# Optimization experiments

Measured on AMD Instinct MI355X. Metric: run time of the kernel, lower is better.

The kernel has to match this reference:

```python
import jax, jax.numpy as jnp
import numpy as np

B, S, H, V, T, NS, NB, NSW = 16, 200, 400, 25000, 8, 30, 3, 36


def setup_inputs() -> dict:
    key = jax.random.key(0)
    ks = jax.random.split(key, 12)
    return {
        "encoded_hidden": jax.random.normal(ks[0], (1, B, H), jnp.float32),
        "encoded_outputs": jax.random.normal(ks[1], (B, S, H), jnp.float32),
        "story": jax.random.randint(ks[2], (B, S), 0, V),
        "target_batches": jax.random.randint(ks[3], (B, NS, T), 0, V),
        "slot_dom_idx": jax.random.randint(ks[4], (NS,), 0, NSW),
        "slot_slot_idx": jax.random.randint(ks[5], (NS,), 0, NSW),
        "emb_W": jax.random.normal(ks[6], (V, H), jnp.float32) * 0.05,
        "slot_emb_W": jax.random.normal(ks[7], (NSW, H), jnp.float32) * 0.1,
        "gru_W_ih": jax.random.normal(ks[8], (3 * H, H), jnp.float32) * 0.05,
        "gru_W_hh": jax.random.normal(ks[9], (3 * H, H), jnp.float32) * 0.05,
        "gru_b_ih": jnp.zeros((3 * H,), jnp.float32),
        "gru_b_hh": jnp.zeros((3 * H,), jnp.float32),
        "W_ratio_w": jax.random.normal(ks[10], (1, 3 * H), jnp.float32) * 0.05,
        "W_ratio_b": jnp.zeros((1,), jnp.float32),
        "W_gate_w": jax.random.normal(ks[11], (NB, H), jnp.float32) * 0.05,
        "W_gate_b": jnp.zeros((NB,), jnp.float32),
    }


def reference(encoded_hidden, encoded_outputs, story, target_batches,
              slot_dom_idx, slot_slot_idx, emb_W, slot_emb_W,
              gru_W_ih, gru_W_hh, gru_b_ih, gru_b_hh,
              W_ratio_w, W_ratio_b, W_gate_w, W_gate_b):
    b, s, h = encoded_outputs.shape
    ns = slot_dom_idx.shape[0]
    v = emb_W.shape[0]
    t = target_batches.shape[2]
    bs = ns * b  # flattened slot*batch dim (parallel decode over slots)

    # slot embedding = domain_emb + slot_emb, broadcast over batch
    slot_emb = slot_emb_W[slot_dom_idx] + slot_emb_W[slot_slot_idx]        # [ns,h]
    dec_in0 = jnp.broadcast_to(slot_emb[:, None, :], (ns, b, h)).reshape(bs, h)
    h0 = jnp.tile(encoded_hidden[0], (ns, 1))                              # [bs,h]
    enc = jnp.tile(encoded_outputs, (ns, 1, 1))                            # [bs,s,h]
    pad_mask = jnp.tile(story == 0, (ns, 1))                               # [bs,s]
    story_rep = jnp.tile(story, (ns, 1))                                   # [bs,s]
    # teacher forcing targets, slot-major flatten: [bs, t]
    tf = jnp.transpose(target_batches, (1, 0, 2)).reshape(bs, t)
    rows = jnp.arange(bs)

    def gru_cell(x, hid):
        gx = x @ gru_W_ih.T + gru_b_ih
        gh = hid @ gru_W_hh.T + gru_b_hh
        r = jax.nn.sigmoid(gx[:, :h] + gh[:, :h])
        z = jax.nn.sigmoid(gx[:, h:2 * h] + gh[:, h:2 * h])
        n = jnp.tanh(gx[:, 2 * h:] + r * gh[:, 2 * h:])
        return (1.0 - z) * n + z * hid

    def step(carry, tgt_t):
        hid, x = carry
        hid = gru_cell(x, hid)                                             # [bs,h]
        scores = jnp.einsum('bh,bsh->bs', hid, enc)
        scores = jnp.where(pad_mask, -jnp.inf, scores)
        prob = jax.nn.softmax(scores, axis=1)                              # [bs,s]
        ctx = jnp.einsum('bs,bsh->bh', prob, enc)                          # [bs,h]
        p_vocab = jax.nn.softmax(hid @ emb_W.T, axis=1)                    # [bs,v]
        switch = jax.nn.sigmoid(
            jnp.concatenate([hid, ctx, x], axis=-1) @ W_ratio_w.T + W_ratio_b)  # [bs,1]
        p_ctx = jnp.zeros((bs, v), p_vocab.dtype).at[rows[:, None], story_rep].add(prob)
        final = (1.0 - switch) * p_ctx + switch * p_vocab                  # [bs,v]
        x_next = emb_W[tgt_t]                                              # teacher forcing
        return (hid, x_next), (final, ctx)

    (_, _), (finals, ctxs) = jax.lax.scan(step, (h0, dec_in0), tf.T)
    all_point = jnp.transpose(finals.reshape(t, ns, b, v), (1, 2, 0, 3))   # [ns,b,t,v]
    all_gate = (ctxs[0] @ W_gate_w.T + W_gate_b).reshape(ns, b, -1)        # [ns,b,nb_gate]
    return all_point, all_gate
```

## Files before the change

### kernel.cpp

```cpp
#include <hip/hip_runtime.h>
#include <math.h>

#define B_   16
#define S_   200
#define H_   400
#define V_   25000
#define T_   8
#define NS_  30
#define NB_  3
#define NSW_ 36
#define BS_  480

#define KP_  448
#define MP_  512
#define NP_  25088
#define NG_  1280
#define MA_  3840
#define NVT_ (NP_/128)
#define PSL_ 200

typedef unsigned short u16;
typedef __attribute__((ext_vector_type(4))) float f32x4;
typedef __attribute__((ext_vector_type(8))) short short8;

__device__ __forceinline__ u16 f2bf(float f) {
    unsigned u = __float_as_uint(f);
    u += 0x7FFFu + ((u >> 16) & 1u);
    return (u16)(u >> 16);
}
__device__ __forceinline__ float bf2f(u16 v) {
    return __uint_as_float(((unsigned)v) << 16);
}
__device__ __forceinline__ float wred_sum(float v) {
    v += __shfl_xor(v, 32); v += __shfl_xor(v, 16); v += __shfl_xor(v, 8);
    v += __shfl_xor(v, 4);  v += __shfl_xor(v, 2);  v += __shfl_xor(v, 1);
    return v;
}
__device__ __forceinline__ float wred_max(float v) {
    v = fmaxf(v, __shfl_xor(v, 32)); v = fmaxf(v, __shfl_xor(v, 16));
    v = fmaxf(v, __shfl_xor(v, 8));  v = fmaxf(v, __shfl_xor(v, 4));
    v = fmaxf(v, __shfl_xor(v, 2));  v = fmaxf(v, __shfl_xor(v, 1));
    return v;
}

__device__ __forceinline__ void gload_lds16(const void* g, void* l) {
    __builtin_amdgcn_global_load_lds(
        (const __attribute__((address_space(1))) void*)g,
        (__attribute__((address_space(3))) void*)l, 16, 0, 0);
}

#define MFMA_SETUP()                                                          \
    const int wid = tid >> 6, lane = tid & 63;                                \
    const int wr = wid >> 1, wc = wid & 1;                                    \
    f32x4 acc[4][4] = {};                                                     \
    const int sslot = lane & 7;                                               \
    const int srow8 = (lane >> 3) & 7;                                        \
    const int lcol = (sslot ^ srow8) * 8;                                     \
    const int lr = lane & 15, lg = lane >> 4, lx = lane & 7;                  \
    const int sA0 = (lg ^ lx) * 8, sA1 = ((4 + lg) ^ lx) * 8;

#define STAGE_TILE(k0_)                                                       \
    {                                                                         \
        _Pragma("unroll")                                                     \
        for (int is = 0; is < 4; ++is) {                                      \
            gload_lds16(Ag + (size_t)is * 8 * KP_ + (k0_),                    \
                        &As[(wid * 32 + is * 8) * 64]);                       \
            gload_lds16(Bg + (size_t)is * 8 * KP_ + (k0_),                    \
                        &Bs[(wid * 32 + is * 8) * 64]);                       \
        }                                                                     \
    }

#define COMPUTE_TILE()                                                        \
    {                                                                         \
        short8 af[4][2], bfr[4][2];                                           \
        _Pragma("unroll")                                                     \
        for (int i = 0; i < 4; ++i) {                                         \
            int ra = (wr * 64 + i * 16 + lr) * 64;                            \
            af[i][0] = *reinterpret_cast<const short8*>(&As[ra + sA0]);       \
            af[i][1] = *reinterpret_cast<const short8*>(&As[ra + sA1]);       \
            int rb = (wc * 64 + i * 16 + lr) * 64;                            \
            bfr[i][0] = *reinterpret_cast<const short8*>(&Bs[rb + sA0]);      \
            bfr[i][1] = *reinterpret_cast<const short8*>(&Bs[rb + sA1]);      \
        }                                                                     \
        _Pragma("unroll")                                                     \
        for (int h = 0; h < 2; ++h)                                           \
            _Pragma("unroll")                                                 \
            for (int i = 0; i < 4; ++i)                                       \
                _Pragma("unroll")                                             \
                for (int j = 0; j < 4; ++j)                                   \
                    acc[i][j] = __builtin_amdgcn_mfma_f32_16x16x32_bf16(      \
                        af[i][h], bfr[j][h], acc[i][j], 0, 0, 0);             \
    }

#define MFMA_KLOOP_SB()                                                       \
    _Pragma("unroll")                                                         \
    for (int kt = 0; kt < 7; ++kt) {                                          \
        STAGE_TILE(kt * 64);                                                  \
        __syncthreads();                                                      \
        COMPUTE_TILE();                                                       \
        __syncthreads();                                                      \
    }

__global__ void init_all(const float* __restrict__ eh, float* __restrict__ hid,
                         u16* __restrict__ Ab) {
    int i = blockIdx.x * blockDim.x + threadIdx.x;
    if (i >= MP_ * KP_) return;
    int row = i / KP_, d = i - row * KP_;
    u16 v = 0;
    if (row < BS_ && d < H_) {
        float h = eh[(row % B_) * H_ + d];
        hid[row * H_ + d] = h;
        v = f2bf(h);
    }
    Ab[i] = v;
}

__device__ __forceinline__ void conv_chunk(const float* __restrict__ src,
                                           u16* __restrict__ dst, int i, int rows) {
    int row = i / (KP_ / 8), c8 = (i - row * (KP_ / 8)) * 8;
    short8 o = {};
    if (row < rows && c8 < H_) {
        const float4* s = reinterpret_cast<const float4*>(src + (size_t)row * H_ + c8);
        float4 a = s[0], b = s[1];
        o[0] = (short)f2bf(a.x); o[1] = (short)f2bf(a.y);
        o[2] = (short)f2bf(a.z); o[3] = (short)f2bf(a.w);
        o[4] = (short)f2bf(b.x); o[5] = (short)f2bf(b.y);
        o[6] = (short)f2bf(b.z); o[7] = (short)f2bf(b.w);
    }
    *reinterpret_cast<short8*>(dst + (size_t)row * KP_ + c8) = o;
}

__global__ void conv_all(const float* __restrict__ embW, const float* __restrict__ Wih,
                         const float* __restrict__ Whh, u16* __restrict__ Bb,
                         u16* __restrict__ Wihb, u16* __restrict__ Whhb) {
    const int CB = NP_ * (KP_ / 8), CG = NG_ * (KP_ / 8);
    int i = blockIdx.x * blockDim.x + threadIdx.x;
    if (i < CB) conv_chunk(embW, Bb, i, V_);
    else if (i < CB + CG) conv_chunk(Wih, Wihb, i - CB, 3 * H_);
    else if (i < CB + 2 * CG) conv_chunk(Whh, Whhb, i - CB - CG, 3 * H_);
}

__global__ void xall_prep(const int* __restrict__ tb, const float* __restrict__ embW,
                          const float* __restrict__ sembW,
                          const int* __restrict__ dom, const int* __restrict__ sli,
                          float* __restrict__ x_all, u16* __restrict__ Xb_all) {
    int i = blockIdx.x * blockDim.x + threadIdx.x;
    if (i >= MA_ * (KP_ / 8)) return;
    int row = i / (KP_ / 8), c8 = (i - row * (KP_ / 8)) * 8;
    int t = row / BS_, r = row - t * BS_;
    int batch = r % B_, slot = r / B_;
    short8 o = {};
    if (c8 < H_) {
        float4 a, b;
        if (t == 0) {
            const float4* s0 = reinterpret_cast<const float4*>(sembW + dom[slot] * H_ + c8);
            const float4* s1 = reinterpret_cast<const float4*>(sembW + sli[slot] * H_ + c8);
            float4 x0 = s0[0], x1 = s0[1], y0 = s1[0], y1 = s1[1];
            a = make_float4(x0.x + y0.x, x0.y + y0.y, x0.z + y0.z, x0.w + y0.w);
            b = make_float4(x1.x + y1.x, x1.y + y1.y, x1.z + y1.z, x1.w + y1.w);
        } else {
            int tok = tb[(batch * NS_ + slot) * T_ + (t - 1)];
            const float4* s = reinterpret_cast<const float4*>(embW + (size_t)tok * H_ + c8);
            a = s[0]; b = s[1];
        }
        o[0] = (short)f2bf(a.x); o[1] = (short)f2bf(a.y);
        o[2] = (short)f2bf(a.z); o[3] = (short)f2bf(a.w);
        o[4] = (short)f2bf(b.x); o[5] = (short)f2bf(b.y);
        o[6] = (short)f2bf(b.z); o[7] = (short)f2bf(b.w);
        *reinterpret_cast<float4*>(x_all + (size_t)row * H_ + c8) = a;
        *reinterpret_cast<float4*>(x_all + (size_t)row * H_ + c8 + 4) = b;
    }
    *reinterpret_cast<short8*>(Xb_all + (size_t)row * KP_ + c8) = o;
}

__global__ __launch_bounds__(256)
void gemm_setup(const u16* __restrict__ Xb_all, const u16* __restrict__ Abuf,
                const u16* __restrict__ Wihb, const u16* __restrict__ Whhb,
                float* __restrict__ gx_all, float* __restrict__ gh) {
    __shared__ u16 As[128 * 64];
    __shared__ u16 Bs[128 * 64];
    const int tid = threadIdx.x;
    const bool mainp = blockIdx.y < (MA_ / 128);
    const int m0 = (mainp ? blockIdx.y : blockIdx.y - MA_ / 128) * 128;
    const int n0 = blockIdx.x * 128;
    const u16* A = mainp ? Xb_all : Abuf;
    const u16* Bw = mainp ? Wihb : Whhb;
    float* C = mainp ? gx_all : gh;
    const int Mlim = mainp ? MA_ : BS_;

    MFMA_SETUP();
    const u16* Ag = A + (size_t)(m0 + wid * 32 + (lane >> 3)) * KP_ + lcol;
    const u16* Bg = Bw + (size_t)(n0 + wid * 32 + (lane >> 3)) * KP_ + lcol;
    MFMA_KLOOP_SB();

    const int m_base = m0 + wr * 64 + lg * 4;
    const int n_base = n0 + wc * 64 + lr;
    #pragma unroll
    for (int i = 0; i < 4; ++i)
        #pragma unroll
        for (int r = 0; r < 4; ++r) {
            int m = m_base + i * 16 + r;
            if (m >= Mlim) continue;
            #pragma unroll
            for (int j = 0; j < 4; ++j) {
                int n = n_base + j * 16;
                if (n < 3 * H_) C[(size_t)m * 3 * H_ + n] = acc[i][j][r];
            }
        }
}

__global__ __launch_bounds__(256, 2)
void vocab_gh(const u16* __restrict__ A, const u16* __restrict__ Bb,
              const u16* __restrict__ Whhb, u16* __restrict__ pb,
              float* __restrict__ psum, float* __restrict__ gh) {
    __shared__ u16 As[256 * 64];
    __shared__ u16 Bs[128 * 64];
    __shared__ float sred[2][256];
    const int bid = blockIdx.x;
    const int tid = threadIdx.x;
    const int xcd = bid & 7, idx = bid >> 3;
    const int lin = (xcd < 4) ? (xcd * 52 + idx) : (208 + (xcd - 4) * 51 + idx);
    const int ntall = lin >> 1, mt = lin & 1;
    const bool isv = (ntall < NVT_);
    const int n0 = (isv ? ntall : ntall - NVT_) * 128;
    const int m0 = mt * 256;
    const u16* Bsrc = isv ? Bb : Whhb;

    const int wid = tid >> 6, lane = tid & 63;
    const int wr = wid >> 1, wc = wid & 1;
    f32x4 acc[8][4] = {};
    const int sslot = lane & 7;
    const int srow8 = (lane >> 3) & 7;
    const int lcol = (sslot ^ srow8) * 8;
    const int lr = lane & 15, lg = lane >> 4, lx = lane & 7;
    const int sA0 = (lg ^ lx) * 8, sA1 = ((4 + lg) ^ lx) * 8;

    const u16* Ag = A + (size_t)(m0 + wid * 64 + (lane >> 3)) * KP_ + lcol;
    const u16* Bg = Bsrc + (size_t)(n0 + wid * 32 + (lane >> 3)) * KP_ + lcol;

    for (int kt = 0; kt < 7; ++kt) {
        const int k0 = kt * 64;
        #pragma unroll
        for (int is = 0; is < 8; ++is)
            gload_lds16(Ag + (size_t)is * 8 * KP_ + k0, &As[(wid * 64 + is * 8) * 64]);
        #pragma unroll
        for (int is = 0; is < 4; ++is)
            gload_lds16(Bg + (size_t)is * 8 * KP_ + k0, &Bs[(wid * 32 + is * 8) * 64]);
        __syncthreads();
        #pragma unroll
        for (int h = 0; h < 2; ++h) {
            const int sA = h ? sA1 : sA0;
            short8 af[8], bf[4];
            #pragma unroll
            for (int i = 0; i < 8; ++i)
                af[i] = *reinterpret_cast<const short8*>(&As[(wr * 128 + i * 16 + lr) * 64 + sA]);
            #pragma unroll
            for (int j = 0; j < 4; ++j)
                bf[j] = *reinterpret_cast<const short8*>(&Bs[(wc * 64 + j * 16 + lr) * 64 + sA]);
            #pragma unroll
            for (int i = 0; i < 8; ++i)
                #pragma unroll
                for (int j = 0; j < 4; ++j)
                    acc[i][j] = __builtin_amdgcn_mfma_f32_16x16x32_bf16(
                        af[i], bf[j], acc[i][j], 0, 0, 0);
        }
        __syncthreads();
    }

    const int m_base = m0 + wr * 128 + lg * 4;
    const int n_base = n0 + wc * 64 + lr;
    if (isv) {
        #pragma unroll
        for (int i = 0; i < 8; ++i) {
            #pragma unroll
            for (int r = 0; r < 4; ++r) {
                int m = m_base + i * 16 + r;
                float js = 0.f;
                #pragma unroll
                for (int j = 0; j < 4; ++j) {
                    int n = n_base + j * 16;
                    float e = __expf(acc[i][j][r]);
                    if (m < BS_ && n < V_) {
                        pb[(size_t)m * V_ + n] = f2bf(e);
                        js += e;
                    }
                }
                js += __shfl_xor(js, 1);
                js += __shfl_xor(js, 2);
                js += __shfl_xor(js, 4);
                js += __shfl_xor(js, 8);
                if ((lane & 15) == 0) sred[wc][m - m0] = js;
            }
        }
        __syncthreads();
        {
            int m = m0 + tid;
            psum[(size_t)m * PSL_ + ntall] = sred[0][tid] + sred[1][tid];
        }
    } else {
        #pragma unroll
        for (int i = 0; i < 8; ++i)
            #pragma unroll
            for (int r = 0; r < 4; ++r) {
                int m = m_base + i * 16 + r;
                if (m >= BS_) continue;
                #pragma unroll
                for (int j = 0; j < 4; ++j) {
                    int n = n_base + j * 16;
                    if (n < 3 * H_) gh[(size_t)m * 3 * H_ + n] = acc[i][j][r];
                }
            }
    }
}

__global__ __launch_bounds__(256)
void attn_fin(const float* __restrict__ gx_all, const float* __restrict__ gh,
              const float* __restrict__ bih, const float* __restrict__ bhh,
              float* __restrict__ hid, u16* __restrict__ Ab,
              const float* __restrict__ x_all,
              const float* __restrict__ enc, const int* __restrict__ story,
              const float* __restrict__ Wr, const float* __restrict__ Wrb,
              const float* __restrict__ Wg, const float* __restrict__ Wgb,
              float* __restrict__ prob_cur, float* __restrict__ sw_cur,
              float* __restrict__ gate_out,
              float* __restrict__ out, const u16* __restrict__ pb,
              const float* __restrict__ psum, const float* __restrict__ sw_prev,
              const float* __restrict__ prob_prev, int t) {
    const int bid = blockIdx.x;
    const int lin = (bid & 7) * 120 + (bid >> 3);
    const int work = lin >> 1, kind = lin & 1;
    const int tid = threadIdx.x, w = tid >> 6, l = tid & 63;
    __shared__ __align__(16) float hs[H_];
    __shared__ __align__(16) float xs[H_];
    __shared__ __align__(16) float cs[H_];
    __shared__ float sc[S_];
    __shared__ float red[16];

    if (kind == 1) {
        if (t == 0) return;
        const int row = work, batch = row % B_;
        float rs = (tid < NVT_) ? psum[(size_t)row * PSL_ + tid] : 0.f;
        rs = wred_sum(rs);
        if (l == 0) red[w] = rs;
        __syncthreads();
        float denom = red[0] + red[1] + red[2] + red[3];
        float swv = sw_prev[row];
        float scl = swv / denom;
        const u16* ps = pb + (size_t)row * V_;
        float* p = out + ((size_t)row * T_ + (t - 1)) * V_;
        for (int v = tid * 8; v < V_; v += 256 * 8) {
            short8 in = *reinterpret_cast<const short8*>(ps + v);
            float4 o0, o1;
            o0.x = bf2f((u16)in[0]) * scl; o0.y = bf2f((u16)in[1]) * scl;
            o0.z = bf2f((u16)in[2]) * scl; o0.w = bf2f((u16)in[3]) * scl;
            o1.x = bf2f((u16)in[4]) * scl; o1.y = bf2f((u16)in[5]) * scl;
            o1.z = bf2f((u16)in[6]) * scl; o1.w = bf2f((u16)in[7]) * scl;
            *reinterpret_cast<float4*>(p + v) = o0;
            *reinterpret_cast<float4*>(p + v + 4) = o1;
        }
        __syncthreads();
        float om = 1.f - swv;
        for (int s = tid; s < S_; s += 256) {
            int tok = story[batch * S_ + s];
            atomicAdd(p + tok, om * prob_prev[(size_t)row * S_ + s]);
        }
        return;
    }

    const int batch = work / 30, slot = work - batch * 30;
    const int row = slot * B_ + batch;

    const float* gxr = gx_all + ((size_t)t * BS_ + row) * 3 * H_;
    const float* ghr = gh + (size_t)row * 3 * H_;
    const float* xr  = x_all + ((size_t)t * BS_ + row) * H_;
    for (int d = tid; d < H_; d += 256) {
        float r = 1.f / (1.f + expf(-(gxr[d] + bih[d] + ghr[d] + bhh[d])));
        float z = 1.f / (1.f + expf(-(gxr[H_ + d] + bih[H_ + d] + ghr[H_ + d] + bhh[H_ + d])));
        float n = tanhf(gxr[2 * H_ + d] + bih[2 * H_ + d] + r * (ghr[2 * H_ + d] + bhh[2 * H_ + d]));
        float h = (1.f - z) * n + z * hid[(size_t)row * H_ + d];
        hs[d] = h;
        hid[(size_t)row * H_ + d] = h;
        Ab[(size_t)row * KP_ + d] = f2bf(h);
        xs[d] = xr[d];
    }
    __syncthreads();

    const float* encb = enc + (size_t)batch * S_ * H_;
    {
        float4 hv1 = *reinterpret_cast<const float4*>(&hs[l * 4]);
        float4 hv2 = make_float4(0.f, 0.f, 0.f, 0.f);
        if (l < 36) hv2 = *reinterpret_cast<const float4*>(&hs[256 + l * 4]);
        for (int k = 0; k < 50; ++k) {
            int s = w * 50 + k;
            const float4* e = reinterpret_cast<const float4*>(encb + (size_t)s * H_);
            float4 ev = e[l];
            float part = ev.x * hv1.x + ev.y * hv1.y + ev.z * hv1.z + ev.w * hv1.w;
            if (l < 36) {
                float4 ev2 = e[64 + l];
                part += ev2.x * hv2.x + ev2.y * hv2.y + ev2.z * hv2.z + ev2.w * hv2.w;
            }
            part = wred_sum(part);
            if (l == 0)
                sc[s] = (story[batch * S_ + s] == 0) ? -1e30f : part;
        }
    }
    __syncthreads();

    float v = (tid < S_) ? sc[tid] : -1e30f;
    float wm = wred_max(v);
    if (l == 0) red[w] = wm;
    __syncthreads();
    float mx = fmaxf(fmaxf(red[0], red[1]), fmaxf(red[2], red[3]));
    float e = (tid < S_) ? __expf(v - mx) : 0.f;
    float wsum = wred_sum(e);
    if (l == 0) red[4 + w] = wsum;
    __syncthreads();
    float inv = 1.f / (red[4] + red[5] + red[6] + red[7]);
    if (tid < S_) {
        float pv = e * inv;
        sc[tid] = pv;
        prob_cur[(size_t)row * S_ + tid] = pv;
    }
    __syncthreads();

    for (int d = tid; d < H_; d += 256) {
        float a0 = 0.f, a1 = 0.f;
        for (int s = 0; s < S_; s += 2) {
            a0 += sc[s] * encb[(size_t)s * H_ + d];
            a1 += sc[s + 1] * encb[(size_t)(s + 1) * H_ + d];
        }
        cs[d] = a0 + a1;
    }
    __syncthreads();

    float part = 0.f;
    for (int i = tid; i < 3 * H_; i += 256) {
        float xv = (i < H_) ? hs[i] : (i < 2 * H_) ? cs[i - H_] : xs[i - 2 * H_];
        part += xv * Wr[i];
    }
    part = wred_sum(part);
    if (l == 0) red[8 + w] = part;
    __syncthreads();
    if (tid == 0)
        sw_cur[row] = 1.f / (1.f + expf(-(red[8] + red[9] + red[10] + red[11] + Wrb[0])));

    if (t == 0 && tid < NB_) {
        float acc = 0.f;
        for (int d = 0; d < H_; ++d) acc += cs[d] * Wg[tid * H_ + d];
        gate_out[(size_t)row * NB_ + tid] = acc + Wgb[tid];
    }
}

__global__ __launch_bounds__(256)
void scale_scatter(float* __restrict__ out, const u16* __restrict__ pb,
                   const float* __restrict__ psum, const float* __restrict__ sw,
                   const float* __restrict__ prob, const int* __restrict__ story) {
    const int row = blockIdx.x;
    const int tid = threadIdx.x, w = tid >> 6, l = tid & 63;
    __shared__ float red[4];
    float rs = (tid < NVT_) ? psum[(size_t)row * PSL_ + tid] : 0.f;
    rs = wred_sum(rs);
    if (l == 0) red[w] = rs;
    __syncthreads();
    float denom = red[0] + red[1] + red[2] + red[3];
    float swv = sw[row];
    float scl = swv / denom;
    const u16* ps = pb + (size_t)row * V_;
    float* p = out + ((size_t)row * T_ + (T_ - 1)) * V_;
    for (int v = tid * 8; v < V_; v += 256 * 8) {
        short8 in = *reinterpret_cast<const short8*>(ps + v);
        float4 o0, o1;
        o0.x = bf2f((u16)in[0]) * scl; o0.y = bf2f((u16)in[1]) * scl;
        o0.z = bf2f((u16)in[2]) * scl; o0.w = bf2f((u16)in[3]) * scl;
        o1.x = bf2f((u16)in[4]) * scl; o1.y = bf2f((u16)in[5]) * scl;
        o1.z = bf2f((u16)in[6]) * scl; o1.w = bf2f((u16)in[7]) * scl;
        *reinterpret_cast<float4*>(p + v) = o0;
        *reinterpret_cast<float4*>(p + v + 4) = o1;
    }
    __syncthreads();
    const int batch = row % B_;
    float om = 1.f - swv;
    for (int s = tid; s < S_; s += 256) {
        int tok = story[batch * S_ + s];
        atomicAdd(p + tok, om * prob[(size_t)row * S_ + s]);
    }
}

extern "C" void kernel_launch(void* const* d_in, const int* in_sizes, int n_in,
                              void* d_out, int out_size, void* d_ws, size_t ws_size,
                              hipStream_t stream) {
    const float* eh    = (const float*)d_in[0];
    const float* enc   = (const float*)d_in[1];
    const int*   story = (const int*)d_in[2];
    const int*   tb    = (const int*)d_in[3];
    const int*   dom   = (const int*)d_in[4];
    const int*   sli   = (const int*)d_in[5];
    const float* embW  = (const float*)d_in[6];
    const float* sembW = (const float*)d_in[7];
    const float* Wih   = (const float*)d_in[8];
    const float* Whh   = (const float*)d_in[9];
    const float* bih   = (const float*)d_in[10];
    const float* bhh   = (const float*)d_in[11];
    const float* Wr    = (const float*)d_in[12];
    const float* Wrb   = (const float*)d_in[13];
    const float* Wg    = (const float*)d_in[14];
    const float* Wgb   = (const float*)d_in[15];

    float* out = (float*)d_out;
    float* ws  = (float*)d_ws;

    float* gx_all = ws;
    float* gh     = gx_all + (size_t)MA_ * 3 * H_;
    float* hid    = gh + (size_t)BS_ * 3 * H_;
    float* x_all  = hid + (size_t)BS_ * H_;
    float* prob2  = x_all + (size_t)MA_ * H_;
    float* sw2    = prob2 + 2 * BS_ * S_;
    float* psum   = sw2 + 2 * BS_;
    u16* Ab     = (u16*)(psum + (size_t)MP_ * PSL_);
    u16* Xb_all = Ab + (size_t)MP_ * KP_;
    u16* Wihb   = Xb_all + (size_t)MA_ * KP_;
    u16* Whhb   = Wihb + (size_t)NG_ * KP_;
    u16* Bb     = Whhb + (size_t)NG_ * KP_;
    u16* pb     = Bb + (size_t)NP_ * KP_;
    size_t need = (size_t)((char*)(pb + (size_t)BS_ * V_) - (char*)ws);
    if (ws_size < need) return;

    float* gate_out = out + (size_t)NS_ * B_ * T_ * V_;

    init_all<<<(MP_ * KP_ + 255) / 256, 256, 0, stream>>>(eh, hid, Ab);
    {
        int tot = (NP_ + 2 * NG_) * (KP_ / 8);
        conv_all<<<(tot + 255) / 256, 256, 0, stream>>>(embW, Wih, Whh, Bb, Wihb, Whhb);
    }
    xall_prep<<<(MA_ * (KP_ / 8) + 255) / 256, 256, 0, stream>>>(tb, embW, sembW, dom, sli,
                                                                 x_all, Xb_all);
    gemm_setup<<<dim3(NG_ / 128, MA_ / 128 + MP_ / 128), 256, 0, stream>>>(
        Xb_all, Ab, Wihb, Whhb, gx_all, gh);

    for (int t = 0; t < T_; ++t) {
        const int cur = t & 1, prev = cur ^ 1;
        attn_fin<<<960, 256, 0, stream>>>(gx_all, gh, bih, bhh, hid, Ab, x_all,
                                          enc, story, Wr, Wrb, Wg, Wgb,
                                          prob2 + cur * BS_ * S_, sw2 + cur * BS_,
                                          gate_out, out, pb, psum,
                                          sw2 + prev * BS_, prob2 + prev * BS_ * S_, t);
        vocab_gh<<<412, 256, 0, stream>>>(Ab, Bb, Whhb, pb, psum, gh);
    }
    {
        const int last = (T_ - 1) & 1;
        scale_scatter<<<BS_, 256, 0, stream>>>(out, pb, psum, sw2 + last * BS_,
                                               prob2 + last * BS_ * S_, story);
    }
}
```

Baseline: 777.9 us.

## Fuse decode loop into persistent cooperative kernel with grid syncs

Replaces the per-step attn_fin/vocab_gh launches with one cooperative persistent kernel that runs the setup GEMM, the attention step and the vocab GEMM, separated by grid-wide syncs. Setup conversion kernels are merged into one prep kernel. The finalize/scatter of the previous step now runs alongside the vocab GEMM using double-buffered pb/psum. The aim is to cut kernel launch overhead and idle tails between steps, at the cost of grid-sync latency and limited occupancy for 512 co-resident blocks. A non-cooperative fallback path keeps separate launches.

```diff
diff --git a/kernel.cpp b/kernel.cpp
--- a/kernel.cpp
+++ b/kernel.cpp
@@ -1,5 +1,8 @@
 #include <hip/hip_runtime.h>
+#include <hip/hip_cooperative_groups.h>
 #include <math.h>
+
+namespace cg = cooperative_groups;
 
 #define B_   16
 #define S_   200
@@ -8,7 +11,6 @@
 #define T_   8
 #define NS_  30
 #define NB_  3
-#define NSW_ 36
 #define BS_  480
 
 #define KP_  448
@@ -18,6 +20,8 @@
 #define MA_  3840
 #define NVT_ (NP_/128)
 #define PSL_ 200
+#define GRID_ 512
+#define SMEM_ 51200
 
 typedef unsigned short u16;
 typedef __attribute__((ext_vector_type(4))) float f32x4;
@@ -42,157 +46,62 @@
     v = fmaxf(v, __shfl_xor(v, 2));  v = fmaxf(v, __shfl_xor(v, 1));
     return v;
 }
-
 __device__ __forceinline__ void gload_lds16(const void* g, void* l) {
     __builtin_amdgcn_global_load_lds(
         (const __attribute__((address_space(1))) void*)g,
         (__attribute__((address_space(3))) void*)l, 16, 0, 0);
 }
 
-#define MFMA_SETUP()                                                          \
-    const int wid = tid >> 6, lane = tid & 63;                                \
-    const int wr = wid >> 1, wc = wid & 1;                                    \
-    f32x4 acc[4][4] = {};                                                     \
-    const int sslot = lane & 7;                                               \
-    const int srow8 = (lane >> 3) & 7;                                        \
-    const int lcol = (sslot ^ srow8) * 8;                                     \
-    const int lr = lane & 15, lg = lane >> 4, lx = lane & 7;                  \
-    const int sA0 = (lg ^ lx) * 8, sA1 = ((4 + lg) ^ lx) * 8;
-
-#define STAGE_TILE(k0_)                                                       \
-    {                                                                         \
-        _Pragma("unroll")                                                     \
-        for (int is = 0; is < 4; ++is) {                                      \
-            gload_lds16(Ag + (size_t)is * 8 * KP_ + (k0_),                    \
-                        &As[(wid * 32 + is * 8) * 64]);                       \
-            gload_lds16(Bg + (size_t)is * 8 * KP_ + (k0_),                    \
-                        &Bs[(wid * 32 + is * 8) * 64]);                       \
-        }                                                                     \
-    }
-
-#define COMPUTE_TILE()                                                        \
-    {                                                                         \
-        short8 af[4][2], bfr[4][2];                                           \
-        _Pragma("unroll")                                                     \
-        for (int i = 0; i < 4; ++i) {                                         \
-            int ra = (wr * 64 + i * 16 + lr) * 64;                            \
-            af[i][0] = *reinterpret_cast<const short8*>(&As[ra + sA0]);       \
-            af[i][1] = *reinterpret_cast<const short8*>(&As[ra + sA1]);       \
-            int rb = (wc * 64 + i * 16 + lr) * 64;                            \
-            bfr[i][0] = *reinterpret_cast<const short8*>(&Bs[rb + sA0]);      \
-            bfr[i][1] = *reinterpret_cast<const short8*>(&Bs[rb + sA1]);      \
-        }                                                                     \
-        _Pragma("unroll")                                                     \
-        for (int h = 0; h < 2; ++h)                                           \
-            _Pragma("unroll")                                                 \
-            for (int i = 0; i < 4; ++i)                                       \
-                _Pragma("unroll")                                             \
-                for (int j = 0; j < 4; ++j)                                   \
-                    acc[i][j] = __builtin_amdgcn_mfma_f32_16x16x32_bf16(      \
-                        af[i][h], bfr[j][h], acc[i][j], 0, 0, 0);             \
-    }
-
-#define MFMA_KLOOP_SB()                                                       \
-    _Pragma("unroll")                                                         \
-    for (int kt = 0; kt < 7; ++kt) {                                          \
-        STAGE_TILE(kt * 64);                                                  \
-        __syncthreads();                                                      \
-        COMPUTE_TILE();                                                       \
-        __syncthreads();                                                      \
-    }
-
-__global__ void init_all(const float* __restrict__ eh, float* __restrict__ hid,
-                         u16* __restrict__ Ab) {
-    int i = blockIdx.x * blockDim.x + threadIdx.x;
-    if (i >= MP_ * KP_) return;
-    int row = i / KP_, d = i - row * KP_;
-    u16 v = 0;
-    if (row < BS_ && d < H_) {
-        float h = eh[(row % B_) * H_ + d];
-        hid[row * H_ + d] = h;
-        v = f2bf(h);
-    }
-    Ab[i] = v;
-}
-
-__device__ __forceinline__ void conv_chunk(const float* __restrict__ src,
-                                           u16* __restrict__ dst, int i, int rows) {
-    int row = i / (KP_ / 8), c8 = (i - row * (KP_ / 8)) * 8;
-    short8 o = {};
-    if (row < rows && c8 < H_) {
-        const float4* s = reinterpret_cast<const float4*>(src + (size_t)row * H_ + c8);
-        float4 a = s[0], b = s[1];
-        o[0] = (short)f2bf(a.x); o[1] = (short)f2bf(a.y);
-        o[2] = (short)f2bf(a.z); o[3] = (short)f2bf(a.w);
-        o[4] = (short)f2bf(b.x); o[5] = (short)f2bf(b.y);
-        o[6] = (short)f2bf(b.z); o[7] = (short)f2bf(b.w);
-    }
-    *reinterpret_cast<short8*>(dst + (size_t)row * KP_ + c8) = o;
-}
-
-__global__ void conv_all(const float* __restrict__ embW, const float* __restrict__ Wih,
-                         const float* __restrict__ Whh, u16* __restrict__ Bb,
-                         u16* __restrict__ Wihb, u16* __restrict__ Whhb) {
-    const int CB = NP_ * (KP_ / 8), CG = NG_ * (KP_ / 8);
-    int i = blockIdx.x * blockDim.x + threadIdx.x;
-    if (i < CB) conv_chunk(embW, Bb, i, V_);
-    else if (i < CB + CG) conv_chunk(Wih, Wihb, i - CB, 3 * H_);
-    else if (i < CB + 2 * CG) conv_chunk(Whh, Whhb, i - CB - CG, 3 * H_);
-}
-
-__global__ void xall_prep(const int* __restrict__ tb, const float* __restrict__ embW,
-                          const float* __restrict__ sembW,
-                          const int* __restrict__ dom, const int* __restrict__ sli,
-                          float* __restrict__ x_all, u16* __restrict__ Xb_all) {
-    int i = blockIdx.x * blockDim.x + threadIdx.x;
-    if (i >= MA_ * (KP_ / 8)) return;
-    int row = i / (KP_ / 8), c8 = (i - row * (KP_ / 8)) * 8;
-    int t = row / BS_, r = row - t * BS_;
-    int batch = r % B_, slot = r / B_;
-    short8 o = {};
-    if (c8 < H_) {
-        float4 a, b;
-        if (t == 0) {
-            const float4* s0 = reinterpret_cast<const float4*>(sembW + dom[slot] * H_ + c8);
-            const float4* s1 = reinterpret_cast<const float4*>(sembW + sli[slot] * H_ + c8);
-            float4 x0 = s0[0], x1 = s0[1], y0 = s1[0], y1 = s1[1];
-            a = make_float4(x0.x + y0.x, x0.y + y0.y, x0.z + y0.z, x0.w + y0.w);
-            b = make_float4(x1.x + y1.x, x1.y + y1.y, x1.z + y1.z, x1.w + y1.w);
-        } else {
-            int tok = tb[(batch * NS_ + slot) * T_ + (t - 1)];
-            const float4* s = reinterpret_cast<const float4*>(embW + (size_t)tok * H_ + c8);
-            a = s[0]; b = s[1];
-        }
-        o[0] = (short)f2bf(a.x); o[1] = (short)f2bf(a.y);
-        o[2] = (short)f2bf(a.z); o[3] = (short)f2bf(a.w);
-        o[4] = (short)f2bf(b.x); o[5] = (short)f2bf(b.y);
-        o[6] = (short)f2bf(b.z); o[7] = (short)f2bf(b.w);
-        *reinterpret_cast<float4*>(x_all + (size_t)row * H_ + c8) = a;
-        *reinterpret_cast<float4*>(x_all + (size_t)row * H_ + c8 + 4) = b;
-    }
-    *reinterpret_cast<short8*>(Xb_all + (size_t)row * KP_ + c8) = o;
-}
-
-__global__ __launch_bounds__(256)
-void gemm_setup(const u16* __restrict__ Xb_all, const u16* __restrict__ Abuf,
-                const u16* __restrict__ Wihb, const u16* __restrict__ Whhb,
-                float* __restrict__ gx_all, float* __restrict__ gh) {
-    __shared__ u16 As[128 * 64];
-    __shared__ u16 Bs[128 * 64];
-    const int tid = threadIdx.x;
-    const bool mainp = blockIdx.y < (MA_ / 128);
-    const int m0 = (mainp ? blockIdx.y : blockIdx.y - MA_ / 128) * 128;
-    const int n0 = blockIdx.x * 128;
+__device__ __forceinline__ void setup_item(int item, const u16* Xb_all, const u16* Abuf,
+        const u16* Wihb, const u16* Whhb, float* gx_all, float* gh, char* smem, int tid) {
+    u16* As = (u16*)smem;
+    u16* Bs = (u16*)(smem + 16384);
+    const int nt = item % 10, mtile = item / 10;
+    const bool mainp = mtile < (MA_ / 128);
+    const int m0 = (mainp ? mtile : mtile - MA_ / 128) * 128;
+    const int n0 = nt * 128;
     const u16* A = mainp ? Xb_all : Abuf;
     const u16* Bw = mainp ? Wihb : Whhb;
     float* C = mainp ? gx_all : gh;
     const int Mlim = mainp ? MA_ : BS_;
 
-    MFMA_SETUP();
+    const int wid = tid >> 6, lane = tid & 63;
+    const int wr = wid >> 1, wc = wid & 1;
+    f32x4 acc[4][4] = {};
+    const int lcol = ((lane & 7) ^ ((lane >> 3) & 7)) * 8;
+    const int lr = lane & 15, lg = lane >> 4, lx = lane & 7;
+    const int sA0 = (lg ^ lx) * 8, sA1 = ((4 + lg) ^ lx) * 8;
     const u16* Ag = A + (size_t)(m0 + wid * 32 + (lane >> 3)) * KP_ + lcol;
     const u16* Bg = Bw + (size_t)(n0 + wid * 32 + (lane >> 3)) * KP_ + lcol;
-    MFMA_KLOOP_SB();
-
+
+    for (int kt = 0; kt < 7; ++kt) {
+        const int k0 = kt * 64;
+        #pragma unroll
+        for (int is = 0; is < 4; ++is) {
+            gload_lds16(Ag + (size_t)is * 8 * KP_ + k0, &As[(wid * 32 + is * 8) * 64]);
+            gload_lds16(Bg + (size_t)is * 8 * KP_ + k0, &Bs[(wid * 32 + is * 8) * 64]);
+        }
+        __syncthreads();
+        short8 af[4][2], bfr[4][2];
+        #pragma unroll
+        for (int i = 0; i < 4; ++i) {
+            int ra = (wr * 64 + i * 16 + lr) * 64;
+            af[i][0] = *reinterpret_cast<const short8*>(&As[ra + sA0]);
+            af[i][1] = *reinterpret_cast<const short8*>(&As[ra + sA1]);
+            int rb = (wc * 64 + i * 16 + lr) * 64;
+            bfr[i][0] = *reinterpret_cast<const short8*>(&Bs[rb + sA0]);
+            bfr[i][1] = *reinterpret_cast<const short8*>(&Bs[rb + sA1]);
+        }
+        #pragma unroll
+        for (int h = 0; h < 2; ++h)
+            #pragma unroll
+            for (int i = 0; i < 4; ++i)
+                #pragma unroll
+                for (int j = 0; j < 4; ++j)
+                    acc[i][j] = __builtin_amdgcn_mfma_f32_16x16x32_bf16(
+                        af[i][h], bfr[j][h], acc[i][j], 0, 0, 0);
+        __syncthreads();
+    }
     const int m_base = m0 + wr * 64 + lg * 4;
     const int n_base = n0 + wc * 64 + lr;
     #pragma unroll
@@ -209,16 +118,12 @@
         }
 }
 
-__global__ __launch_bounds__(256, 2)
-void vocab_gh(const u16* __restrict__ A, const u16* __restrict__ Bb,
-              const u16* __restrict__ Whhb, u16* __restrict__ pb,
-              float* __restrict__ psum, float* __restrict__ gh) {
-    __shared__ u16 As[256 * 64];
-    __shared__ u16 Bs[128 * 64];
-    __shared__ float sred[2][256];
-    const int bid = blockIdx.x;
-    const int tid = threadIdx.x;
-    const int xcd = bid & 7, idx = bid >> 3;
+__device__ __forceinline__ void vocab_item(int vbid, const u16* A, const u16* Bb,
+        const u16* Whhb, u16* pb, float* psum, float* gh, char* smem, int tid) {
+    u16* As = (u16*)smem;
+    u16* Bs = (u16*)(smem + 32768);
+    float (*sred)[256] = (float (*)[256])(smem + 49152);
+    const int xcd = vbid & 7, idx = vbid >> 3;
     const int lin = (xcd < 4) ? (xcd * 52 + idx) : (208 + (xcd - 4) * 51 + idx);
     const int ntall = lin >> 1, mt = lin & 1;
     const bool isv = (ntall < NVT_);
@@ -229,12 +134,9 @@
     const int wid = tid >> 6, lane = tid & 63;
     const int wr = wid >> 1, wc = wid & 1;
     f32x4 acc[8][4] = {};
-    const int sslot = lane & 7;
-    const int srow8 = (lane >> 3) & 7;
-    const int lcol = (sslot ^ srow8) * 8;
+    const int lcol = ((lane & 7) ^ ((lane >> 3) & 7)) * 8;
     const int lr = lane & 15, lg = lane >> 4, lx = lane & 7;
     const int sA0 = (lg ^ lx) * 8, sA1 = ((4 + lg) ^ lx) * 8;
-
     const u16* Ag = A + (size_t)(m0 + wid * 64 + (lane >> 3)) * KP_ + lcol;
     const u16* Bg = Bsrc + (size_t)(n0 + wid * 32 + (lane >> 3)) * KP_ + lcol;
 
@@ -313,62 +215,53 @@
     }
 }
 
-__global__ __launch_bounds__(256)
-void attn_fin(const float* __restrict__ gx_all, const float* __restrict__ gh,
-              const float* __restrict__ bih, const float* __restrict__ bhh,
-              float* __restrict__ hid, u16* __restrict__ Ab,
-              const float* __restrict__ x_all,
-              const float* __restrict__ enc, const int* __restrict__ story,
-              const float* __restrict__ Wr, const float* __restrict__ Wrb,
-              const float* __restrict__ Wg, const float* __restrict__ Wgb,
-              float* __restrict__ prob_cur, float* __restrict__ sw_cur,
-              float* __restrict__ gate_out,
-              float* __restrict__ out, const u16* __restrict__ pb,
-              const float* __restrict__ psum, const float* __restrict__ sw_prev,
-              const float* __restrict__ prob_prev, int t) {
-    const int bid = blockIdx.x;
-    const int lin = (bid & 7) * 120 + (bid >> 3);
-    const int work = lin >> 1, kind = lin & 1;
-    const int tid = threadIdx.x, w = tid >> 6, l = tid & 63;
-    __shared__ __align__(16) float hs[H_];
-    __shared__ __align__(16) float xs[H_];
-    __shared__ __align__(16) float cs[H_];
-    __shared__ float sc[S_];
-    __shared__ float red[16];
-
-    if (kind == 1) {
-        if (t == 0) return;
-        const int row = work, batch = row % B_;
-        float rs = (tid < NVT_) ? psum[(size_t)row * PSL_ + tid] : 0.f;
-        rs = wred_sum(rs);
-        if (l == 0) red[w] = rs;
-        __syncthreads();
-        float denom = red[0] + red[1] + red[2] + red[3];
-        float swv = sw_prev[row];
-        float scl = swv / denom;
-        const u16* ps = pb + (size_t)row * V_;
-        float* p = out + ((size_t)row * T_ + (t - 1)) * V_;
-        for (int v = tid * 8; v < V_; v += 256 * 8) {
-            short8 in = *reinterpret_cast<const short8*>(ps + v);
-            float4 o0, o1;
-            o0.x = bf2f((u16)in[0]) * scl; o0.y = bf2f((u16)in[1]) * scl;
-            o0.z = bf2f((u16)in[2]) * scl; o0.w = bf2f((u16)in[3]) * scl;
-            o1.x = bf2f((u16)in[4]) * scl; o1.y = bf2f((u16)in[5]) * scl;
-            o1.z = bf2f((u16)in[6]) * scl; o1.w = bf2f((u16)in[7]) * scl;
-            *reinterpret_cast<float4*>(p + v) = o0;
-            *reinterpret_cast<float4*>(p + v + 4) = o1;
-        }
-        __syncthreads();
-        float om = 1.f - swv;
-        for (int s = tid; s < S_; s += 256) {
-            int tok = story[batch * S_ + s];
-            atomicAdd(p + tok, om * prob_prev[(size_t)row * S_ + s]);
-        }
-        return;
-    }
-
-    const int batch = work / 30, slot = work - batch * 30;
+__device__ __forceinline__ void fin_row(int row, int tout, float* out, const u16* pb,
+        const float* psum, const float* sw, const float* prob, const int* story,
+        char* smem, int tid) {
+    float* red = (float*)smem;
+    const int w = tid >> 6, l = tid & 63;
+    const int batch = row % B_;
+    float rs = (tid < NVT_) ? psum[(size_t)row * PSL_ + tid] : 0.f;
+    rs = wred_sum(rs);
+    if (l == 0) red[w] = rs;
+    __syncthreads();
+    float denom = red[0] + red[1] + red[2] + red[3];
+    float swv = sw[row];
+    float scl = swv / denom;
+    const u16* ps = pb + (size_t)row * V_;
+    float* p = out + ((size_t)row * T_ + tout) * V_;
+    for (int v = tid * 8; v < V_; v += 256 * 8) {
+        short8 in = *reinterpret_cast<const short8*>(ps + v);
+        float4 o0, o1;
+        o0.x = bf2f((u16)in[0]) * scl; o0.y = bf2f((u16)in[1]) * scl;
+        o0.z = bf2f((u16)in[2]) * scl; o0.w = bf2f((u16)in[3]) * scl;
+        o1.x = bf2f((u16)in[4]) * scl; o1.y = bf2f((u16)in[5]) * scl;
+        o1.z = bf2f((u16)in[6]) * scl; o1.w = bf2f((u16)in[7]) * scl;
+        *reinterpret_cast<float4*>(p + v) = o0;
+        *reinterpret_cast<float4*>(p + v + 4) = o1;
+    }
+    __syncthreads();
+    float om = 1.f - swv;
+    for (int s = tid; s < S_; s += 256) {
+        int tok = story[batch * S_ + s];
+        atomicAdd(p + tok, om * prob[(size_t)row * S_ + s]);
+    }
+}
+
+__device__ __forceinline__ void attn_body(int abid, int t,
+        const float* gx_all, const float* gh, const float* bih, const float* bhh,
+        float* hid, u16* Ab, const float* x_all, const float* enc, const int* story,
+        const float* Wr, const float* Wrb, const float* Wg, const float* Wgb,
+        float* prob_cur, float* sw_cur, float* gate_out, char* smem, int tid) {
+    float* hs = (float*)smem;
+    float* xs = (float*)(smem + 1600);
+    float* cs = (float*)(smem + 3200);
+    float* sc = (float*)(smem + 4800);
+    float* red = (float*)(smem + 5600);
+    const int lin = (abid & 7) * 60 + (abid >> 3);
+    const int batch = lin / 30, slot = lin - batch * 30;
     const int row = slot * B_ + batch;
+    const int w = tid >> 6, l = tid & 63;
 
     const float* gxr = gx_all + ((size_t)t * BS_ + row) * 3 * H_;
     const float* ghr = gh + (size_t)row * 3 * H_;
@@ -449,41 +342,153 @@
         for (int d = 0; d < H_; ++d) acc += cs[d] * Wg[tid * H_ + d];
         gate_out[(size_t)row * NB_ + tid] = acc + Wgb[tid];
     }
-}
-
-__global__ __launch_bounds__(256)
-void scale_scatter(float* __restrict__ out, const u16* __restrict__ pb,
-                   const float* __restrict__ psum, const float* __restrict__ sw,
-                   const float* __restrict__ prob, const int* __restrict__ story) {
-    const int row = blockIdx.x;
-    const int tid = threadIdx.x, w = tid >> 6, l = tid & 63;
-    __shared__ float red[4];
-    float rs = (tid < NVT_) ? psum[(size_t)row * PSL_ + tid] : 0.f;
-    rs = wred_sum(rs);
-    if (l == 0) red[w] = rs;
-    __syncthreads();
-    float denom = red[0] + red[1] + red[2] + red[3];
-    float swv = sw[row];
-    float scl = swv / denom;
-    const u16* ps = pb + (size_t)row * V_;
-    float* p = out + ((size_t)row * T_ + (T_ - 1)) * V_;
-    for (int v = tid * 8; v < V_; v += 256 * 8) {
-        short8 in = *reinterpret_cast<const short8*>(ps + v);
-        float4 o0, o1;
-        o0.x = bf2f((u16)in[0]) * scl; o0.y = bf2f((u16)in[1]) * scl;
-        o0.z = bf2f((u16)in[2]) * scl; o0.w = bf2f((u16)in[3]) * scl;
-        o1.x = bf2f((u16)in[4]) * scl; o1.y = bf2f((u16)in[5]) * scl;
-        o1.z = bf2f((u16)in[6]) * scl; o1.w = bf2f((u16)in[7]) * scl;
-        *reinterpret_cast<float4*>(p + v) = o0;
-        *reinterpret_cast<float4*>(p + v + 4) = o1;
-    }
-    __syncthreads();
-    const int batch = row % B_;
-    float om = 1.f - swv;
-    for (int s = tid; s < S_; s += 256) {
-        int tok = story[batch * S_ + s];
-        atomicAdd(p + tok, om * prob[(size_t)row * S_ + s]);
-    }
+    __syncthreads();
+}
+
+__global__ void prep_all(const float* __restrict__ eh, const float* __restrict__ embW,
+                         const float* __restrict__ Wih, const float* __restrict__ Whh,
+                         const float* __restrict__ sembW, const int* __restrict__ tb,
+                         const int* __restrict__ dom, const int* __restrict__ sli,
+                         float* __restrict__ hid, u16* __restrict__ Ab,
+                         u16* __restrict__ Bb, u16* __restrict__ Wihb, u16* __restrict__ Whhb,
+                         float* __restrict__ x_all, u16* __restrict__ Xb_all) {
+    const int R0 = MP_ * KP_;
+    const int CB = NP_ * (KP_ / 8), CG = NG_ * (KP_ / 8);
+    const int R1 = R0 + CB + 2 * CG;
+    const int R2 = R1 + MA_ * (KP_ / 8);
+    int i = blockIdx.x * 256 + threadIdx.x;
+    if (i < R0) {
+        int row = i / KP_, d = i - row * KP_;
+        u16 v = 0;
+        if (row < BS_ && d < H_) {
+            float h = eh[(row % B_) * H_ + d];
+            hid[row * H_ + d] = h;
+            v = f2bf(h);
+        }
+        Ab[i] = v;
+    } else if (i < R1) {
+        int j = i - R0;
+        const float* src; u16* dst; int rows;
+        if (j < CB) { src = embW; dst = Bb; rows = V_; }
+        else if (j < CB + CG) { src = Wih; dst = Wihb; rows = 3 * H_; j -= CB; }
+        else { src = Whh; dst = Whhb; rows = 3 * H_; j -= CB + CG; }
+        int row = j / (KP_ / 8), c8 = (j - row * (KP_ / 8)) * 8;
+        short8 o = {};
+        if (row < rows && c8 < H_) {
+            const float4* s = reinterpret_cast<const float4*>(src + (size_t)row * H_ + c8);
+            float4 a = s[0], b = s[1];
+            o[0] = (short)f2bf(a.x); o[1] = (short)f2bf(a.y);
+            o[2] = (short)f2bf(a.z); o[3] = (short)f2bf(a.w);
+            o[4] = (short)f2bf(b.x); o[5] = (short)f2bf(b.y);
+            o[6] = (short)f2bf(b.z); o[7] = (short)f2bf(b.w);
+        }
+        *reinterpret_cast<short8*>(dst + (size_t)row * KP_ + c8) = o;
+    } else if (i < R2) {
+        int j = i - R1;
+        int row = j / (KP_ / 8), c8 = (j - row * (KP_ / 8)) * 8;
+        int t = row / BS_, r = row - t * BS_;
+        int batch = r % B_, slot = r / B_;
+        short8 o = {};
+        if (c8 < H_) {
+            float4 a, b;
+            if (t == 0) {
+                const float4* s0 = reinterpret_cast<const float4*>(sembW + dom[slot] * H_ + c8);
+                const float4* s1 = reinterpret_cast<const float4*>(sembW + sli[slot] * H_ + c8);
+                float4 x0 = s0[0], x1 = s0[1], y0 = s1[0], y1 = s1[1];
+                a = make_float4(x0.x + y0.x, x0.y + y0.y, x0.z + y0.z, x0.w + y0.w);
+                b = make_float4(x1.x + y1.x, x1.y + y1.y, x1.z + y1.z, x1.w + y1.w);
+            } else {
+                int tok = tb[(batch * NS_ + slot) * T_ + (t - 1)];
+                const float4* s = reinterpret_cast<const float4*>(embW + (size_t)tok * H_ + c8);
+                a = s[0]; b = s[1];
+            }
+            o[0] = (short)f2bf(a.x); o[1] = (short)f2bf(a.y);
+            o[2] = (short)f2bf(a.z); o[3] = (short)f2bf(a.w);
+            o[4] = (short)f2bf(b.x); o[5] = (short)f2bf(b.y);
+            o[6] = (short)f2bf(b.z); o[7] = (short)f2bf(b.w);
+            *reinterpret_cast<float4*>(x_all + (size_t)row * H_ + c8) = a;
+            *reinterpret_cast<float4*>(x_all + (size_t)row * H_ + c8 + 4) = b;
+        }
+        *reinterpret_cast<short8*>(Xb_all + (size_t)row * KP_ + c8) = o;
+    }
+}
+
+struct P {
+    const float *gx_all_c; float *gx_all, *gh, *hid, *x_all, *prob2, *sw2, *psum2, *gate_out, *out;
+    const float *bih, *bhh, *enc, *Wr, *Wrb, *Wg, *Wgb;
+    const int *story;
+    u16 *Ab, *pb0, *pb1;
+    const u16 *Xb_all, *Wihb, *Whhb, *Bb;
+};
+
+__global__ __launch_bounds__(256, 2) void persist(P p) {
+    cg::grid_group gg = cg::this_grid();
+    __shared__ __align__(16) char smem[SMEM_];
+    const int bid = blockIdx.x, tid = threadIdx.x;
+
+    for (int item = bid; item < 340; item += GRID_)
+        setup_item(item, p.Xb_all, p.Ab, p.Wihb, p.Whhb, p.gx_all, p.gh, smem, tid);
+    gg.sync();
+
+    for (int t = 0; t < T_; ++t) {
+        const int cur = t & 1, prev = cur ^ 1;
+        if (bid < BS_)
+            attn_body(bid, t, p.gx_all, p.gh, p.bih, p.bhh, p.hid, p.Ab, p.x_all,
+                      p.enc, p.story, p.Wr, p.Wrb, p.Wg, p.Wgb,
+                      p.prob2 + cur * BS_ * S_, p.sw2 + cur * BS_, p.gate_out, smem, tid);
+        gg.sync();
+        u16* pb_cur = cur ? p.pb1 : p.pb0;
+        u16* pb_prev = prev ? p.pb1 : p.pb0;
+        for (int item = bid; item < 892; item += GRID_) {
+            if (item < 412)
+                vocab_item(item, p.Ab, p.Bb, p.Whhb, pb_cur,
+                           p.psum2 + (size_t)cur * MP_ * PSL_, p.gh, smem, tid);
+            else if (t > 0)
+                fin_row(item - 412, t - 1, p.out, pb_prev,
+                        p.psum2 + (size_t)prev * MP_ * PSL_, p.sw2 + prev * BS_,
+                        p.prob2 + prev * BS_ * S_, p.story, smem, tid);
+            __syncthreads();
+        }
+        gg.sync();
+    }
+    {
+        const int last = (T_ - 1) & 1;
+        for (int item = bid; item < BS_; item += GRID_)
+            fin_row(item, T_ - 1, p.out, last ? p.pb1 : p.pb0,
+                    p.psum2 + (size_t)last * MP_ * PSL_, p.sw2 + last * BS_,
+                    p.prob2 + last * BS_ * S_, p.story, smem, tid);
+    }
+}
+
+__global__ __launch_bounds__(256) void k_setup(P p) {
+    __shared__ __align__(16) char smem[SMEM_];
+    setup_item(blockIdx.x, p.Xb_all, p.Ab, p.Wihb, p.Whhb, p.gx_all, p.gh, smem, threadIdx.x);
+}
+__global__ __launch_bounds__(256) void k_attn(P p, int t) {
+    __shared__ __align__(16) char smem[8192];
+    const int cur = t & 1;
+    attn_body(blockIdx.x, t, p.gx_all, p.gh, p.bih, p.bhh, p.hid, p.Ab, p.x_all,
+              p.enc, p.story, p.Wr, p.Wrb, p.Wg, p.Wgb,
+              p.prob2 + cur * BS_ * S_, p.sw2 + cur * BS_, p.gate_out, smem, threadIdx.x);
+}
+__global__ __launch_bounds__(256) void k_vocab_fin(P p, int t) {
+    __shared__ __align__(16) char smem[SMEM_];
+    const int cur = t & 1, prev = cur ^ 1;
+    const int bid = blockIdx.x;
+    if (bid < 412)
+        vocab_item(bid, p.Ab, p.Bb, p.Whhb, cur ? p.pb1 : p.pb0,
+                   p.psum2 + (size_t)cur * MP_ * PSL_, p.gh, smem, threadIdx.x);
+    else if (t > 0)
+        fin_row(bid - 412, t - 1, p.out, prev ? p.pb1 : p.pb0,
+                p.psum2 + (size_t)prev * MP_ * PSL_, p.sw2 + prev * BS_,
+                p.prob2 + prev * BS_ * S_, p.story, smem, threadIdx.x);
+}
+__global__ __launch_bounds__(256) void k_fin(P p) {
+    __shared__ __align__(16) char smem[1024];
+    const int last = (T_ - 1) & 1;
+    fin_row(blockIdx.x, T_ - 1, p.out, last ? p.pb1 : p.pb0,
+            p.psum2 + (size_t)last * MP_ * PSL_, p.sw2 + last * BS_,
+            p.prob2 + last * BS_ * S_, p.story, smem, threadIdx.x);
 }
 
 extern "C" void kernel_launch(void* const* d_in, const int* in_sizes, int n_in,
@@ -515,40 +520,47 @@
     float* x_all  = hid + (size_t)BS_ * H_;
     float* prob2  = x_all + (size_t)MA_ * H_;
     float* sw2    = prob2 + 2 * BS_ * S_;
-    float* psum   = sw2 + 2 * BS_;
-    u16* Ab     = (u16*)(psum + (size_t)MP_ * PSL_);
+    float* psum2  = sw2 + 2 * BS_;
+    u16* Ab     = (u16*)(psum2 + 2 * (size_t)MP_ * PSL_);
     u16* Xb_all = Ab + (size_t)MP_ * KP_;
     u16* Wihb   = Xb_all + (size_t)MA_ * KP_;
     u16* Whhb   = Wihb + (size_t)NG_ * KP_;
     u16* Bb     = Whhb + (size_t)NG_ * KP_;
-    u16* pb     = Bb + (size_t)NP_ * KP_;
-    size_t need = (size_t)((char*)(pb + (size_t)BS_ * V_) - (char*)ws);
+    u16* pb0    = Bb + (size_t)NP_ * KP_;
+    u16* pb1    = pb0 + (size_t)BS_ * V_;
+    size_t need = (size_t)((char*)(pb1 + (size_t)BS_ * V_) - (char*)ws);
     if (ws_size < need) return;
 
     float* gate_out = out + (size_t)NS_ * B_ * T_ * V_;
 
-    init_all<<<(MP_ * KP_ + 255) / 256, 256, 0, stream>>>(eh, hid, Ab);
+    P p;
+    p.gx_all = gx_all; p.gh = gh; p.hid = hid; p.x_all = x_all;
+    p.prob2 = prob2; p.sw2 = sw2; p.psum2 = psum2; p.gate_out = gate_out; p.out = out;
+    p.bih = bih; p.bhh = bhh; p.enc = enc; p.Wr = Wr; p.Wrb = Wrb; p.Wg = Wg; p.Wgb = Wgb;
+    p.story = story; p.Ab = Ab; p.pb0 = pb0; p.pb1 = pb1;
+    p.Xb_all = Xb_all; p.Wihb = Wihb; p.Whhb = Whhb; p.Bb = Bb;
+
     {
-        int tot = (NP_ + 2 * NG_) * (KP_ / 8);
-        conv_all<<<(tot + 255) / 256, 256, 0, stream>>>(embW, Wih, Whh, Bb, Wihb, Whhb);
-    }
-    xall_prep<<<(MA_ * (KP_ / 8) + 255) / 256, 256, 0, stream>>>(tb, embW, sembW, dom, sli,
-                                                                 x_all, Xb_all);
-    gemm_setup<<<dim3(NG_ / 128, MA_ / 128 + MP_ / 128), 256, 0, stream>>>(
-        Xb_all, Ab, Wihb, Whhb, gx_all, gh);
-
-    for (int t = 0; t < T_; ++t) {
-        const int cur = t & 1, prev = cur ^ 1;
-        attn_fin<<<960, 256, 0, stream>>>(gx_all, gh, bih, bhh, hid, Ab, x_all,
-                                          enc, story, Wr, Wrb, Wg, Wgb,
-                                          prob2 + cur * BS_ * S_, sw2 + cur * BS_,
-                                          gate_out, out, pb, psum,
-                                          sw2 + prev * BS_, prob2 + prev * BS_ * S_, t);
-        vocab_gh<<<412, 256, 0, stream>>>(Ab, Bb, Whhb, pb, psum, gh);
-    }
-    {
-        const int last = (T_ - 1) & 1;
-        scale_scatter<<<BS_, 256, 0, stream>>>(out, pb, psum, sw2 + last * BS_,
-                                               prob2 + last * BS_ * S_, story);
-    }
-}
+        const int R2 = MP_ * KP_ + (NP_ + 2 * NG_) * (KP_ / 8) + MA_ * (KP_ / 8);
+        prep_all<<<(R2 + 255) / 256, 256, 0, stream>>>(eh, embW, Wih, Whh, sembW, tb, dom, sli,
+                                                       hid, Ab, Bb, Wihb, Whhb, x_all, Xb_all);
+    }
+
+    int nb = 0;
+    bool coop = (hipOccupancyMaxActiveBlocksPerMultiprocessor(&nb, (const void*)persist, 256, 0)
+                 == hipSuccess) && (nb >= 2);
+    if (coop) {
+        void* kargs[] = { &p };
+        if (hipLaunchCooperativeKernel((const void*)persist, dim3(GRID_), dim3(256),
+                                       kargs, 0, stream) != hipSuccess)
+            coop = false;
+    }
+    if (!coop) {
+        k_setup<<<340, 256, 0, stream>>>(p);
+        for (int t = 0; t < T_; ++t) {
+            k_attn<<<BS_, 256, 0, stream>>>(p, t);
+            k_vocab_fin<<<892, 256, 0, stream>>>(p, t);
+        }
+        k_fin<<<BS_, 256, 0, stream>>>(p);
+    }
+}
```

Result: slower. 986.9 us (+26.9%).
